# Kernel optimization log

Hardware: AMD Instinct MI355X
Metric: run time of the kernel (lower is better)

## Reference

```python
import jax, jax.numpy as jnp
import numpy as np

NEG_INF = float(np.finfo(np.float32).min)


def setup_inputs() -> dict:
    key = jax.random.key(0)
    k1, k2, k3 = jax.random.split(key, 3)
    n_context, d_model = 4096, 2048
    x = jax.random.normal(k1, (n_context, d_model), dtype=jnp.float32)
    # nn.Linear default init scale ~ 1/sqrt(fan_in); use small weights for numeric sanity
    W_qk = jax.random.normal(k2, (d_model, d_model), dtype=jnp.float32) / np.sqrt(d_model)
    W_ov = jax.random.normal(k3, (d_model, d_model), dtype=jnp.float32) / np.sqrt(d_model)
    return {"x": x, "W_qk": W_qk, "W_ov": W_ov}


def reference(x, W_qk, W_ov):
    # Faithful to: softmax(X @ W_qk.T @ X.T + causal_mask) @ X @ W_ov.T
    # (biases of the torch Linears are never used in forward)
    n = x.shape[0]
    q = x @ W_qk.T                      # [n, d]
    scores = q @ x.T                    # [n, n]  (no 1/sqrt(d) scaling, as in source)
    causal = jnp.tril(jnp.ones((n, n), dtype=bool))
    scores = jnp.where(causal, scores, NEG_INF)  # additive -inf mask equivalent
    attn = jax.nn.softmax(scores, axis=-1)       # [n, n]
    out = (attn @ x) @ W_ov.T                    # [n, d]
    return out
```

## Files before the change

kernel.cpp:

```cpp
#include <hip/hip_runtime.h>
#include <hip/hip_bf16.h>
#include <stdint.h>
#include <stddef.h>
#include <math.h>

typedef _Float16 f16;
typedef __attribute__((ext_vector_type(8))) _Float16 f16x8;
typedef __attribute__((ext_vector_type(4))) float    f32x4;

constexpr int BM = 128, BN = 128, BK = 64;

#define GLOAD_LDS16(gp, lp)                                        \
    __builtin_amdgcn_global_load_lds(                              \
        (const __attribute__((address_space(1))) unsigned int*)(gp),\
        (__attribute__((address_space(3))) unsigned int*)(lp), 16, 0, 0)

#define MFMA_TILE(AV, BV)                                                     \
    do {                                                                      \
        __builtin_amdgcn_s_setprio(1);                                        \
        _Pragma("unroll")                                                     \
        for (int mi_ = 0; mi_ < 4; ++mi_)                                     \
            _Pragma("unroll")                                                 \
            for (int ni_ = 0; ni_ < 4; ++ni_)                                 \
                acc[mi_][ni_] = __builtin_amdgcn_mfma_f32_16x16x32_f16(       \
                    (AV)[mi_], (BV)[ni_], acc[mi_][ni_], 0, 0, 0);            \
        __builtin_amdgcn_s_setprio(0);                                        \
    } while (0)

template <int EPI>
__global__ __launch_bounds__(512, 2) void gemm8_a2(
    const f16* __restrict__ Ah, const f16* __restrict__ Al,
    const f16* __restrict__ B,
    float* __restrict__ Cf, f16* __restrict__ Co, f16* __restrict__ Clo,
    int M, int N, int K)
{
    const int bx = blockIdx.x;
    const int by = blockIdx.y;

    const int tid   = threadIdx.x;
    const int lane  = tid & 63;
    const int wave  = tid >> 6;
    const int wm    = wave >> 2;
    const int wn    = wave & 3;
    const int lrow  = lane & 15;
    const int lquad = lane >> 4;

    __shared__ f16 lds[2][32768];

    const int row0 = by * 128;
    const int col0 = bx * 256;

    const int srow = tid >> 3;
    const int scol = ((tid & 7) ^ (srow & 7)) * 8;
    const int loff = wave * 512;

    const int g0 = ((lquad)     ^ (lrow & 7)) * 8;
    const int g1 = ((4 + lquad) ^ (lrow & 7)) * 8;

    const int arow = (wm * 64 + lrow) * 64;
    const int brow = (wn * 64 + lrow) * 64 + 16384;

    const f16* gAh = Ah + (size_t)(row0 + srow) * K + scol;
    const f16* gAl = Al + (size_t)(row0 + srow) * K + scol;
    const f16* gB  = B  + (size_t)(col0 + srow) * K + scol;
    const size_t r64 = (size_t)64 * K;

    f32x4 acc[4][4];
    const f32x4 fz = {0.f, 0.f, 0.f, 0.f};
    #pragma unroll
    for (int i = 0; i < 4; ++i)
        #pragma unroll
        for (int j = 0; j < 4; ++j) acc[i][j] = fz;

    const int nt = K / 64;

    #pragma unroll
    for (int u = 0; u < 4; ++u)
        GLOAD_LDS16(gB + u * r64, &lds[0][16384 + u * 4096 + loff]);
    #pragma unroll
    for (int u = 0; u < 2; ++u)
        GLOAD_LDS16(gAh + u * r64, &lds[0][u * 4096 + loff]);
    #pragma unroll
    for (int u = 0; u < 2; ++u)
        GLOAD_LDS16(gAl + u * r64, &lds[0][8192 + u * 4096 + loff]);
    asm volatile("s_waitcnt vmcnt(0)");
    __builtin_amdgcn_s_barrier();

    for (int t = 0; t < nt; ++t) {
        const f16* bufc = &lds[t & 1][0];
        f16* bufn = &lds[(t + 1) & 1][0];
        const bool stage = (t + 1 < nt);
        const size_t kn = (size_t)(t + 1) * 64;

        f16x8 ah0[4], ah1[4], al0[4], al1[4], bv0[4], bv1[4];

        #pragma unroll
        for (int mi = 0; mi < 4; ++mi)
            ah0[mi] = *(const f16x8*)&bufc[arow + mi * 1024 + g0];
        #pragma unroll
        for (int ni = 0; ni < 4; ++ni)
            bv0[ni] = *(const f16x8*)&bufc[brow + ni * 1024 + g0];
        #pragma unroll
        for (int mi = 0; mi < 4; ++mi)
            ah1[mi] = *(const f16x8*)&bufc[arow + mi * 1024 + g1];
        #pragma unroll
        for (int ni = 0; ni < 4; ++ni)
            bv1[ni] = *(const f16x8*)&bufc[brow + ni * 1024 + g1];
        #pragma unroll
        for (int mi = 0; mi < 4; ++mi)
            al0[mi] = *(const f16x8*)&bufc[8192 + arow + mi * 1024 + g0];
        #pragma unroll
        for (int mi = 0; mi < 4; ++mi)
            al1[mi] = *(const f16x8*)&bufc[8192 + arow + mi * 1024 + g1];

        if (stage) {
            GLOAD_LDS16(gB + kn,           &bufn[16384 + loff]);
            GLOAD_LDS16(gB + r64 + kn,     &bufn[16384 +  4096 + loff]);
            GLOAD_LDS16(gB + 2 * r64 + kn, &bufn[16384 +  8192 + loff]);
            GLOAD_LDS16(gB + 3 * r64 + kn, &bufn[16384 + 12288 + loff]);
            GLOAD_LDS16(gAh + kn,          &bufn[loff]);
            GLOAD_LDS16(gAh + r64 + kn,    &bufn[4096 + loff]);
            GLOAD_LDS16(gAl + kn,          &bufn[ 8192 + loff]);
            GLOAD_LDS16(gAl + r64 + kn,    &bufn[12288 + loff]);
        }

        MFMA_TILE(ah0, bv0);
        MFMA_TILE(ah1, bv1);
        MFMA_TILE(al0, bv0);
        MFMA_TILE(al1, bv1);

        asm volatile("s_waitcnt vmcnt(0)");
        __builtin_amdgcn_s_barrier();
    }

    #pragma unroll
    for (int mi = 0; mi < 4; ++mi) {
        #pragma unroll
        for (int ni = 0; ni < 4; ++ni) {
            #pragma unroll
            for (int r = 0; r < 4; ++r) {
                const int row = row0 + wm * 64 + mi * 16 + lquad * 4 + r;
                const int col = col0 + wn * 64 + ni * 16 + lrow;
                const size_t idx = (size_t)row * N + col;
                const float v = acc[mi][ni][r];
                if (EPI == 0) {
                    Cf[idx] = v;
                } else {
                    const f16 h = (f16)v;
                    Co[idx]  = h;
                    Clo[idx] = (f16)(v - (float)h);
                }
            }
        }
    }
}

__global__ __launch_bounds__(512, 2) void gemm8_s_jobs(
    const f16* __restrict__ Ah, const f16* __restrict__ Al,
    const f16* __restrict__ B,
    float* __restrict__ Cf, int N, int K)
{
    const int b = blockIdx.x;
    const int j = (b & 7) * 32 + (b >> 3);
    int r = (int)sqrtf((float)j);
    while (r * r > j) --r;
    while ((r + 1) * (r + 1) <= j) ++r;
    const int u = j - r * r;
    const int by = (u < r) ? 2 * r : 2 * r + 1;
    const int bx = (u < r) ? u : u - r;

    const int tid   = threadIdx.x;
    const int lane  = tid & 63;
    const int wave  = tid >> 6;
    const int wm    = wave >> 2;
    const int wn    = wave & 3;
    const int lrow  = lane & 15;
    const int lquad = lane >> 4;

    __shared__ f16 lds[2][32768];

    const int row0 = by * 128;
    const int col0 = bx * 256;

    const int srow = tid >> 3;
    const int scol = ((tid & 7) ^ (srow & 7)) * 8;
    const int loff = wave * 512;

    const int g0 = ((lquad)     ^ (lrow & 7)) * 8;
    const int g1 = ((4 + lquad) ^ (lrow & 7)) * 8;

    const int arow = (wm * 64 + lrow) * 64;
    const int brow = (wn * 64 + lrow) * 64 + 16384;

    const f16* gAh = Ah + (size_t)(row0 + srow) * K + scol;
    const f16* gAl = Al + (size_t)(row0 + srow) * K + scol;
    const f16* gB  = B  + (size_t)(col0 + srow) * K + scol;
    const size_t r64 = (size_t)64 * K;

    f32x4 acc[4][4];
    const f32x4 fz = {0.f, 0.f, 0.f, 0.f};
    #pragma unroll
    for (int i = 0; i < 4; ++i)
        #pragma unroll
        for (int jj = 0; jj < 4; ++jj) acc[i][jj] = fz;

    const int nt = K / 64;

    #pragma unroll
    for (int u2 = 0; u2 < 4; ++u2)
        GLOAD_LDS16(gB + u2 * r64, &lds[0][16384 + u2 * 4096 + loff]);
    #pragma unroll
    for (int u2 = 0; u2 < 2; ++u2)
        GLOAD_LDS16(gAh + u2 * r64, &lds[0][u2 * 4096 + loff]);
    #pragma unroll
    for (int u2 = 0; u2 < 2; ++u2)
        GLOAD_LDS16(gAl + u2 * r64, &lds[0][8192 + u2 * 4096 + loff]);
    asm volatile("s_waitcnt vmcnt(0)");
    __builtin_amdgcn_s_barrier();

    for (int t = 0; t < nt; ++t) {
        const f16* bufc = &lds[t & 1][0];
        f16* bufn = &lds[(t + 1) & 1][0];
        const bool stage = (t + 1 < nt);
        const size_t kn = (size_t)(t + 1) * 64;

        f16x8 ah0[4], ah1[4], al0[4], al1[4], bv0[4], bv1[4];

        #pragma unroll
        for (int mi = 0; mi < 4; ++mi)
            ah0[mi] = *(const f16x8*)&bufc[arow + mi * 1024 + g0];
        #pragma unroll
        for (int ni = 0; ni < 4; ++ni)
            bv0[ni] = *(const f16x8*)&bufc[brow + ni * 1024 + g0];
        #pragma unroll
        for (int mi = 0; mi < 4; ++mi)
            ah1[mi] = *(const f16x8*)&bufc[arow + mi * 1024 + g1];
        #pragma unroll
        for (int ni = 0; ni < 4; ++ni)
            bv1[ni] = *(const f16x8*)&bufc[brow + ni * 1024 + g1];
        #pragma unroll
        for (int mi = 0; mi < 4; ++mi)
            al0[mi] = *(const f16x8*)&bufc[8192 + arow + mi * 1024 + g0];
        #pragma unroll
        for (int mi = 0; mi < 4; ++mi)
            al1[mi] = *(const f16x8*)&bufc[8192 + arow + mi * 1024 + g1];

        if (stage) {
            GLOAD_LDS16(gB + kn,           &bufn[16384 + loff]);
            GLOAD_LDS16(gB + r64 + kn,     &bufn[16384 +  4096 + loff]);
            GLOAD_LDS16(gB + 2 * r64 + kn, &bufn[16384 +  8192 + loff]);
            GLOAD_LDS16(gB + 3 * r64 + kn, &bufn[16384 + 12288 + loff]);
            GLOAD_LDS16(gAh + kn,          &bufn[loff]);
            GLOAD_LDS16(gAh + r64 + kn,    &bufn[4096 + loff]);
            GLOAD_LDS16(gAl + kn,          &bufn[ 8192 + loff]);
            GLOAD_LDS16(gAl + r64 + kn,    &bufn[12288 + loff]);
        }

        MFMA_TILE(ah0, bv0);
        MFMA_TILE(ah1, bv1);
        MFMA_TILE(al0, bv0);
        MFMA_TILE(al1, bv1);

        asm volatile("s_waitcnt vmcnt(0)");
        __builtin_amdgcn_s_barrier();
    }

    #pragma unroll
    for (int mi = 0; mi < 4; ++mi) {
        #pragma unroll
        for (int ni = 0; ni < 4; ++ni) {
            #pragma unroll
            for (int rr = 0; rr < 4; ++rr) {
                const int row = row0 + wm * 64 + mi * 16 + lquad * 4 + rr;
                const int col = col0 + wn * 64 + ni * 16 + lrow;
                Cf[(size_t)row * N + col] = acc[mi][ni][rr];
            }
        }
    }
}

__global__ __launch_bounds__(256) void gemm_half_splitk(
    const f16* __restrict__ Ah, const f16* __restrict__ Al,
    const f16* __restrict__ B, float* __restrict__ Spart, int Kg)
{
    const int kc = blockIdx.x;
    const int h  = blockIdx.y;
    const int row0 = h * 256;
    const int kbeg = kc * 256;

    const int tid   = threadIdx.x;
    const int lane  = tid & 63;
    const int wave  = tid >> 6;
    const int wm    = wave >> 1;
    const int wn    = wave & 1;
    const int lrow  = lane & 15;
    const int lquad = lane >> 4;

    __shared__ f16 sAh[BM * BK];
    __shared__ f16 sAl[BM * BK];
    __shared__ f16 sB [BM * BK];

    const int srow = tid >> 3;
    const int scol = (((tid & 7) ^ ((tid >> 3) & 7))) * 8;
    const int lbase = wave * 512;

    f32x4 acc[4][4];
    const f32x4 fz = {0.f, 0.f, 0.f, 0.f};
    #pragma unroll
    for (int i = 0; i < 4; ++i)
        #pragma unroll
        for (int jj = 0; jj < 4; ++jj) acc[i][jj] = fz;

    for (int k0 = kbeg; k0 < kbeg + 256; k0 += BK) {
        __syncthreads();
        #pragma unroll
        for (int r = 0; r < 4; ++r) {
            const int trow = srow + 32 * r;
            const size_t ga = (size_t)(row0 + trow) * Kg + k0 + scol;
            const int ldst = lbase + r * 2048;
            GLOAD_LDS16(&Ah[ga], &sAh[ldst]);
            GLOAD_LDS16(&Al[ga], &sAl[ldst]);
            GLOAD_LDS16(&B [ga], &sB [ldst]);
        }
        __syncthreads();

        #pragma unroll
        for (int kk = 0; kk < 2; ++kk) {
            const int grpA = ((kk * 4 + lquad) ^ (lrow & 7)) * 8;
            f16x8 ah[4], al[4], bv[4];
            #pragma unroll
            for (int mi = 0; mi < 4; ++mi) {
                const int off = (wm * 64 + mi * 16 + lrow) * BK + grpA;
                ah[mi] = *reinterpret_cast<const f16x8*>(&sAh[off]);
                al[mi] = *reinterpret_cast<const f16x8*>(&sAl[off]);
            }
            #pragma unroll
            for (int ni = 0; ni < 4; ++ni)
                bv[ni] = *reinterpret_cast<const f16x8*>(
                    &sB[(wn * 64 + ni * 16 + lrow) * BK + grpA]);

            #pragma unroll
            for (int mi = 0; mi < 4; ++mi)
                #pragma unroll
                for (int ni = 0; ni < 4; ++ni) {
                    acc[mi][ni] = __builtin_amdgcn_mfma_f32_16x16x32_f16(
                        ah[mi], bv[ni], acc[mi][ni], 0, 0, 0);
                    acc[mi][ni] = __builtin_amdgcn_mfma_f32_16x16x32_f16(
                        al[mi], bv[ni], acc[mi][ni], 0, 0, 0);
                }
        }
    }

    float* outp = Spart + ((size_t)(kc * 16 + h)) * (128 * 128);
    #pragma unroll
    for (int mi = 0; mi < 4; ++mi) {
        #pragma unroll
        for (int ni = 0; ni < 4; ++ni) {
            #pragma unroll
            for (int r = 0; r < 4; ++r) {
                const int row = wm * 64 + mi * 16 + lquad * 4 + r;
                const int col = wn * 64 + ni * 16 + lrow;
                outp[row * 128 + col] = acc[mi][ni][r];
            }
        }
    }
}

__global__ __launch_bounds__(256) void combine_halves(
    const float* __restrict__ Spart, float* __restrict__ S, int n)
{
    const int h = blockIdx.y;
    const int e = (blockIdx.x * 256 + threadIdx.x) * 4;
    float4 a = *reinterpret_cast<const float4*>(
        &Spart[(size_t)h * (128 * 128) + e]);
    #pragma unroll
    for (int kc = 1; kc < 8; ++kc) {
        const float4 b = *reinterpret_cast<const float4*>(
            &Spart[(size_t)(kc * 16 + h) * (128 * 128) + e]);
        a.x += b.x; a.y += b.y; a.z += b.z; a.w += b.w;
    }
    const int i = e >> 7, jj = e & 127;
    *reinterpret_cast<float4*>(&S[(size_t)(h * 256 + i) * n + h * 256 + jj]) = a;
}

template <int EPI, bool KCAUSAL>
__global__ __launch_bounds__(512, 2) void gemm8_1t(
    const f16* __restrict__ A, const f16* __restrict__ B,
    float* __restrict__ Cf, f16* __restrict__ Co,
    int M, int N, int K)
{
    const int bx = blockIdx.x;
    const int by = KCAUSAL ? ((int)gridDim.y - 1 - (int)blockIdx.y) : blockIdx.y;

    const int tid   = threadIdx.x;
    const int lane  = tid & 63;
    const int wave  = tid >> 6;
    const int wm    = wave >> 2;
    const int wn    = wave & 3;
    const int lrow  = lane & 15;
    const int lquad = lane >> 4;

    __shared__ f16 lds[3][24576];

    const int row0 = by * 128;
    const int col0 = bx * 256;

    const int srow = tid >> 3;
    const int scol = ((tid & 7) ^ (srow & 7)) * 8;
    const int loff = wave * 512;
    const int g0 = ((lquad)     ^ (lrow & 7)) * 8;
    const int g1 = ((4 + lquad) ^ (lrow & 7)) * 8;
    const int arow = (wm * 64 + lrow) * 64;
    const int brow = (wn * 64 + lrow) * 64 + 8192;

    const f16* gA = A + (size_t)(row0 + srow) * K + scol;
    const f16* gB = B + (size_t)(col0 + srow) * K + scol;
    const size_t r64 = (size_t)64 * K;

    f32x4 acc[4][4];
    const f32x4 fz = {0.f, 0.f, 0.f, 0.f};
    #pragma unroll
    for (int i = 0; i < 4; ++i)
        #pragma unroll
        for (int j = 0; j < 4; ++j) acc[i][j] = fz;

    const int Keff = KCAUSAL ? (by + 1) * 128 : K;
    const int nt = Keff / 64;

    #pragma unroll
    for (int tt = 0; tt < 2; ++tt) {
        const size_t kk = (size_t)tt * 64;
        #pragma unroll
        for (int u = 0; u < 4; ++u)
            GLOAD_LDS16(gB + u * r64 + kk, &lds[tt][8192 + u * 4096 + loff]);
        #pragma unroll
        for (int u = 0; u < 2; ++u)
            GLOAD_LDS16(gA + u * r64 + kk, &lds[tt][u * 4096 + loff]);
    }
    asm volatile("s_waitcnt vmcnt(6)");
    __builtin_amdgcn_s_barrier();

    int cur = 0;
    for (int t = 0; t < nt; ++t) {
        const int nb = (cur >= 1) ? (cur - 1) : (cur + 2);
        const bool stage2 = (t + 2 < nt);
        const size_t kn = (size_t)(t + 2) * 64;
        const f16* bufc = &lds[cur][0];
        f16* bufn = &lds[nb][0];

        f16x8 av0[4], av1[4], bv0[4], bv1[4];

        #pragma unroll
        for (int mi = 0; mi < 4; ++mi)
            av0[mi] = *(const f16x8*)&bufc[arow + mi * 1024 + g0];
        #pragma unroll
        for (int ni = 0; ni < 4; ++ni)
            bv0[ni] = *(const f16x8*)&bufc[brow + ni * 1024 + g0];
        #pragma unroll
        for (int mi = 0; mi < 4; ++mi)
            av1[mi] = *(const f16x8*)&bufc[arow + mi * 1024 + g1];
        #pragma unroll
        for (int ni = 0; ni < 4; ++ni)
            bv1[ni] = *(const f16x8*)&bufc[brow + ni * 1024 + g1];

        if (stage2) {
            GLOAD_LDS16(gB + kn,           &bufn[8192 + loff]);
            GLOAD_LDS16(gB + r64 + kn,     &bufn[8192 +  4096 + loff]);
            GLOAD_LDS16(gB + 2 * r64 + kn, &bufn[8192 +  8192 + loff]);
            GLOAD_LDS16(gB + 3 * r64 + kn, &bufn[8192 + 12288 + loff]);
            GLOAD_LDS16(gA + kn,           &bufn[loff]);
            GLOAD_LDS16(gA + r64 + kn,     &bufn[4096 + loff]);
        }

        MFMA_TILE(av0, bv0);
        MFMA_TILE(av1, bv1);

        if (stage2) asm volatile("s_waitcnt vmcnt(6)");
        else        asm volatile("s_waitcnt vmcnt(0)");
        __builtin_amdgcn_s_barrier();

        cur = (cur == 2) ? 0 : cur + 1;
    }

    #pragma unroll
    for (int mi = 0; mi < 4; ++mi) {
        #pragma unroll
        for (int ni = 0; ni < 4; ++ni) {
            #pragma unroll
            for (int r = 0; r < 4; ++r) {
                const int row = row0 + wm * 64 + mi * 16 + lquad * 4 + r;
                const int col = col0 + wn * 64 + ni * 16 + lrow;
                const size_t idx = (size_t)row * N + col;
                const float v = acc[mi][ni][r];
                if (EPI == 0) Cf[idx] = v;
                else          Co[idx] = (f16)v;
            }
        }
    }
}

__global__ __launch_bounds__(256) void split_f32_f16(
    const float* __restrict__ in, f16* __restrict__ hi, f16* __restrict__ lo,
    size_t nelem)
{
    const size_t i = ((size_t)blockIdx.x * 256 + threadIdx.x) * 4;
    if (i >= nelem) return;
    const float4 v = *reinterpret_cast<const float4*>(in + i);
    union { f16 h[4]; ushort4 u; } H, L;
    H.h[0] = (f16)v.x; H.h[1] = (f16)v.y; H.h[2] = (f16)v.z; H.h[3] = (f16)v.w;
    *reinterpret_cast<ushort4*>(hi + i) = H.u;
    if (lo) {
        L.h[0] = (f16)(v.x - (float)H.h[0]);
        L.h[1] = (f16)(v.y - (float)H.h[1]);
        L.h[2] = (f16)(v.z - (float)H.h[2]);
        L.h[3] = (f16)(v.w - (float)H.h[3]);
        *reinterpret_cast<ushort4*>(lo + i) = L.u;
    }
}

__global__ __launch_bounds__(256) void prep_x(
    const float* __restrict__ in, f16* __restrict__ hi, f16* __restrict__ lo,
    f16* __restrict__ tr, int rows, int cols)
{
    __shared__ float tile[32][33];
    const int bx = blockIdx.x;
    const int by = blockIdx.y;
    const int tx = threadIdx.x & 31;
    const int ty = threadIdx.x >> 5;
    #pragma unroll
    for (int r = 0; r < 4; ++r) {
        const int row = by * 32 + ty + 8 * r;
        const int col = bx * 32 + tx;
        const float v = in[(size_t)row * cols + col];
        tile[ty + 8 * r][tx] = v;
        const f16 h = (f16)v;
        hi[(size_t)row * cols + col] = h;
        lo[(size_t)row * cols + col] = (f16)(v - (float)h);
    }
    __syncthreads();
    #pragma unroll
    for (int r = 0; r < 4; ++r)
        tr[(size_t)(bx * 32 + ty + 8 * r) * rows + by * 32 + tx] =
            (f16)tile[tx][ty + 8 * r];
}

__global__ __launch_bounds__(256) void softmax_rows(
    const float* __restrict__ S, f16* __restrict__ P, int n)
{
    const int row = blockIdx.x;
    const int len = row + 1;
    const int padlen = ((row >> 7) + 1) << 7;
    const float* srow = S + (size_t)row * n;
    f16* prow = P + (size_t)row * n;
    const int tid = threadIdx.x;
    const int lane = tid & 63, wave = tid >> 6;
    __shared__ float rowbuf[4096];
    __shared__ float redm[4], reds[4];

    float m = -3.0e38f, s = 0.f;
    for (int j = tid; j < len; j += 256) {
        const float v = srow[j];
        rowbuf[j] = v;
        const float mn = fmaxf(m, v);
        s = s * __expf(m - mn) + __expf(v - mn);
        m = mn;
    }
    #pragma unroll
    for (int off = 32; off; off >>= 1) {
        const float mo = __shfl_xor(m, off, 64);
        const float so = __shfl_xor(s, off, 64);
        const float mn = fmaxf(m, mo);
        s = s * __expf(m - mn) + so * __expf(mo - mn);
        m = mn;
    }
    if (lane == 0) { redm[wave] = m; reds[wave] = s; }
    __syncthreads();
    float M = redm[0], Sm = reds[0];
    #pragma unroll
    for (int w = 1; w < 4; ++w) {
        const float mn = fmaxf(M, redm[w]);
        Sm = Sm * __expf(M - mn) + reds[w] * __expf(redm[w] - mn);
        M = mn;
    }
    const float inv = 1.0f / Sm;

    const f16 z = (f16)0.0f;
    for (int j = tid; j < padlen; j += 256)
        prow[j] = (j < len) ? (f16)(__expf(rowbuf[j] - M) * inv) : z;
}

extern "C" void kernel_launch(void* const* d_in, const int* in_sizes, int n_in,
                              void* d_out, int out_size, void* d_ws, size_t ws_size,
                              hipStream_t stream)
{
    const int n = 4096, d = 2048;
    const float* x   = (const float*)d_in[0];
    const float* Wqk = (const float*)d_in[1];
    const float* Wov = (const float*)d_in[2];
    float* out = (float*)d_out;

    char* ws = (char*)d_ws;
    const size_t MB = 1 << 20;
    f16*   xh   = (f16*)  (ws);
    f16*   xl   = (f16*)  (ws + 16 * MB);
    f16*   Wh   = (f16*)  (ws + 32 * MB);
    f16*   Wovh = (f16*)  (ws + 40 * MB);
    f16*   xTh  = (f16*)  (ws + 48 * MB);
    f16*   qh   = (f16*)  (ws + 64 * MB);
    f16*   ql   = (f16*)  (ws + 80 * MB);
    float* S    = (float*)(ws + 96 * MB);
    float* Sp   = (float*)(ws + 16 * MB);
    f16*   P    = (f16*)  (ws);
    f16*   o    = (f16*)  (ws + 64 * MB);

    const dim3 blk(256);
    const dim3 blk8(512);

    split_f32_f16<<<dim3((d * d) / (256 * 4)), blk, 0, stream>>>(Wqk, Wh, nullptr, (size_t)d * d);
    split_f32_f16<<<dim3((d * d) / (256 * 4)), blk, 0, stream>>>(Wov, Wovh, nullptr, (size_t)d * d);
    prep_x<<<dim3(d / 32, n / 32), blk, 0, stream>>>(x, xh, xl, xTh, n, d);

    gemm8_a2<1><<<dim3(d / 256, n / 128), blk8, 0, stream>>>(
        xh, xl, Wh, nullptr, qh, ql, n, d, d);

    gemm8_s_jobs<<<dim3(256), blk8, 0, stream>>>(qh, ql, xh, S, n, d);
    gemm_half_splitk<<<dim3(8, 16), blk, 0, stream>>>(qh, ql, xh, Sp, d);
    combine_halves<<<dim3(16, 16), blk, 0, stream>>>(Sp, S, n);

    softmax_rows<<<dim3(n), blk, 0, stream>>>(S, P, n);

    gemm8_1t<2, true><<<dim3(d / 256, n / 128), blk8, 0, stream>>>(
        P, xTh, nullptr, o, n, d, n);

    gemm8_1t<0, false><<<dim3(d / 256, n / 128), blk8, 0, stream>>>(
        o, Wovh, out, nullptr, n, d, d);
}
```

Measured before the change: 365.9 us.

## Interleave MFMA with LDS reads, XCD-aware block remap, branchless prefetch

Moves the global-to-LDS prefetch earlier in each K iteration and interleaves the MFMA tiles with the LDS fragment reads. sched_group_barrier hints pin the order of MFMA, DS-read and VMEM instruction groups so loads overlap with matrix math. Workgroup IDs are remapped so consecutive tiles land on the same XCD, aiming for better L2 reuse in the non-causal GEMMs. The staging branch is removed by issuing redundant reloads of the last tile, which costs a little extra memory traffic and assumes the workgroup count is a multiple of 8.

```diff
diff --git a/kernel.cpp b/kernel.cpp
--- a/kernel.cpp
+++ b/kernel.cpp
@@ -27,6 +27,8 @@
         __builtin_amdgcn_s_setprio(0);                                        \
     } while (0)
 
+#define SGB __builtin_amdgcn_sched_group_barrier
+
 template <int EPI>
 __global__ __launch_bounds__(512, 2) void gemm8_a2(
     const f16* __restrict__ Ah, const f16* __restrict__ Al,
@@ -34,8 +36,13 @@
     float* __restrict__ Cf, f16* __restrict__ Co, f16* __restrict__ Clo,
     int M, int N, int K)
 {
-    const int bx = blockIdx.x;
-    const int by = blockIdx.y;
+    const int gx  = gridDim.x;
+    const int nwg = gx * gridDim.y;
+    const int id  = blockIdx.y * gx + blockIdx.x;
+    const int cpx = nwg >> 3;
+    const int j   = (id & 7) * cpx + (id >> 3);
+    const int bx  = j % gx;
+    const int by  = j / gx;
 
     const int tid   = threadIdx.x;
     const int lane  = tid & 63;
@@ -70,7 +77,7 @@
     #pragma unroll
     for (int i = 0; i < 4; ++i)
         #pragma unroll
-        for (int j = 0; j < 4; ++j) acc[i][j] = fz;
+        for (int jj = 0; jj < 4; ++jj) acc[i][jj] = fz;
 
     const int nt = K / 64;
 
@@ -89,8 +96,7 @@
     for (int t = 0; t < nt; ++t) {
         const f16* bufc = &lds[t & 1][0];
         f16* bufn = &lds[(t + 1) & 1][0];
-        const bool stage = (t + 1 < nt);
-        const size_t kn = (size_t)(t + 1) * 64;
+        const size_t kn = (size_t)((t + 1 < nt) ? t + 1 : t) * 64;
 
         f16x8 ah0[4], ah1[4], al0[4], al1[4], bv0[4], bv1[4];
 
@@ -100,34 +106,46 @@
         #pragma unroll
         for (int ni = 0; ni < 4; ++ni)
             bv0[ni] = *(const f16x8*)&bufc[brow + ni * 1024 + g0];
+
+        GLOAD_LDS16(gB + kn,           &bufn[16384 + loff]);
+        GLOAD_LDS16(gB + r64 + kn,     &bufn[16384 +  4096 + loff]);
+        GLOAD_LDS16(gB + 2 * r64 + kn, &bufn[16384 +  8192 + loff]);
+        GLOAD_LDS16(gB + 3 * r64 + kn, &bufn[16384 + 12288 + loff]);
+        GLOAD_LDS16(gAh + kn,          &bufn[loff]);
+        GLOAD_LDS16(gAh + r64 + kn,    &bufn[4096 + loff]);
+        GLOAD_LDS16(gAl + kn,          &bufn[ 8192 + loff]);
+        GLOAD_LDS16(gAl + r64 + kn,    &bufn[12288 + loff]);
+
         #pragma unroll
         for (int mi = 0; mi < 4; ++mi)
             ah1[mi] = *(const f16x8*)&bufc[arow + mi * 1024 + g1];
         #pragma unroll
         for (int ni = 0; ni < 4; ++ni)
             bv1[ni] = *(const f16x8*)&bufc[brow + ni * 1024 + g1];
+
+        MFMA_TILE(ah0, bv0);
+
         #pragma unroll
         for (int mi = 0; mi < 4; ++mi)
             al0[mi] = *(const f16x8*)&bufc[8192 + arow + mi * 1024 + g0];
+
+        MFMA_TILE(ah1, bv1);
+
         #pragma unroll
         for (int mi = 0; mi < 4; ++mi)
             al1[mi] = *(const f16x8*)&bufc[8192 + arow + mi * 1024 + g1];
 
-        if (stage) {
-            GLOAD_LDS16(gB + kn,           &bufn[16384 + loff]);
-            GLOAD_LDS16(gB + r64 + kn,     &bufn[16384 +  4096 + loff]);
-            GLOAD_LDS16(gB + 2 * r64 + kn, &bufn[16384 +  8192 + loff]);
-            GLOAD_LDS16(gB + 3 * r64 + kn, &bufn[16384 + 12288 + loff]);
-            GLOAD_LDS16(gAh + kn,          &bufn[loff]);
-            GLOAD_LDS16(gAh + r64 + kn,    &bufn[4096 + loff]);
-            GLOAD_LDS16(gAl + kn,          &bufn[ 8192 + loff]);
-            GLOAD_LDS16(gAl + r64 + kn,    &bufn[12288 + loff]);
-        }
-
-        MFMA_TILE(ah0, bv0);
-        MFMA_TILE(ah1, bv1);
         MFMA_TILE(al0, bv0);
         MFMA_TILE(al1, bv1);
+
+        SGB(0x100, 8, 0);
+        SGB(0x20,  8, 0);
+        SGB(0x100, 8, 0);
+        SGB(0x8,  16, 0);
+        SGB(0x100, 4, 0);
+        SGB(0x8,  16, 0);
+        SGB(0x100, 4, 0);
+        SGB(0x8,  32, 0);
 
         asm volatile("s_waitcnt vmcnt(0)");
         __builtin_amdgcn_s_barrier();
@@ -221,8 +239,7 @@
     for (int t = 0; t < nt; ++t) {
         const f16* bufc = &lds[t & 1][0];
         f16* bufn = &lds[(t + 1) & 1][0];
-        const bool stage = (t + 1 < nt);
-        const size_t kn = (size_t)(t + 1) * 64;
+        const size_t kn = (size_t)((t + 1 < nt) ? t + 1 : t) * 64;
 
         f16x8 ah0[4], ah1[4], al0[4], al1[4], bv0[4], bv1[4];
 
@@ -232,34 +249,46 @@
         #pragma unroll
         for (int ni = 0; ni < 4; ++ni)
             bv0[ni] = *(const f16x8*)&bufc[brow + ni * 1024 + g0];
+
+        GLOAD_LDS16(gB + kn,           &bufn[16384 + loff]);
+        GLOAD_LDS16(gB + r64 + kn,     &bufn[16384 +  4096 + loff]);
+        GLOAD_LDS16(gB + 2 * r64 + kn, &bufn[16384 +  8192 + loff]);
+        GLOAD_LDS16(gB + 3 * r64 + kn, &bufn[16384 + 12288 + loff]);
+        GLOAD_LDS16(gAh + kn,          &bufn[loff]);
+        GLOAD_LDS16(gAh + r64 + kn,    &bufn[4096 + loff]);
+        GLOAD_LDS16(gAl + kn,          &bufn[ 8192 + loff]);
+        GLOAD_LDS16(gAl + r64 + kn,    &bufn[12288 + loff]);
+
         #pragma unroll
         for (int mi = 0; mi < 4; ++mi)
             ah1[mi] = *(const f16x8*)&bufc[arow + mi * 1024 + g1];
         #pragma unroll
         for (int ni = 0; ni < 4; ++ni)
             bv1[ni] = *(const f16x8*)&bufc[brow + ni * 1024 + g1];
+
+        MFMA_TILE(ah0, bv0);
+
         #pragma unroll
         for (int mi = 0; mi < 4; ++mi)
             al0[mi] = *(const f16x8*)&bufc[8192 + arow + mi * 1024 + g0];
+
+        MFMA_TILE(ah1, bv1);
+
         #pragma unroll
         for (int mi = 0; mi < 4; ++mi)
             al1[mi] = *(const f16x8*)&bufc[8192 + arow + mi * 1024 + g1];
 
-        if (stage) {
-            GLOAD_LDS16(gB + kn,           &bufn[16384 + loff]);
-            GLOAD_LDS16(gB + r64 + kn,     &bufn[16384 +  4096 + loff]);
-            GLOAD_LDS16(gB + 2 * r64 + kn, &bufn[16384 +  8192 + loff]);
-            GLOAD_LDS16(gB + 3 * r64 + kn, &bufn[16384 + 12288 + loff]);
-            GLOAD_LDS16(gAh + kn,          &bufn[loff]);
-            GLOAD_LDS16(gAh + r64 + kn,    &bufn[4096 + loff]);
-            GLOAD_LDS16(gAl + kn,          &bufn[ 8192 + loff]);
-            GLOAD_LDS16(gAl + r64 + kn,    &bufn[12288 + loff]);
-        }
-
-        MFMA_TILE(ah0, bv0);
-        MFMA_TILE(ah1, bv1);
         MFMA_TILE(al0, bv0);
         MFMA_TILE(al1, bv1);
+
+        SGB(0x100, 8, 0);
+        SGB(0x20,  8, 0);
+        SGB(0x100, 8, 0);
+        SGB(0x8,  16, 0);
+        SGB(0x100, 4, 0);
+        SGB(0x8,  16, 0);
+        SGB(0x100, 4, 0);
+        SGB(0x8,  32, 0);
 
         asm volatile("s_waitcnt vmcnt(0)");
         __builtin_amdgcn_s_barrier();
@@ -389,8 +418,19 @@
     float* __restrict__ Cf, f16* __restrict__ Co,
     int M, int N, int K)
 {
-    const int bx = blockIdx.x;
-    const int by = KCAUSAL ? ((int)gridDim.y - 1 - (int)blockIdx.y) : blockIdx.y;
+    int bx, by;
+    if (KCAUSAL) {
+        bx = blockIdx.x;
+        by = (int)gridDim.y - 1 - (int)blockIdx.y;
+    } else {
+        const int gx  = gridDim.x;
+        const int nwg = gx * gridDim.y;
+        const int id  = blockIdx.y * gx + blockIdx.x;
+        const int cpx = nwg >> 3;
+        const int j   = (id & 7) * cpx + (id >> 3);
+        bx = j % gx;
+        by = j / gx;
+    }
 
     const int tid   = threadIdx.x;
     const int lane  = tid & 63;
@@ -422,7 +462,7 @@
     #pragma unroll
     for (int i = 0; i < 4; ++i)
         #pragma unroll
-        for (int j = 0; j < 4; ++j) acc[i][j] = fz;
+        for (int j2 = 0; j2 < 4; ++j2) acc[i][j2] = fz;
 
     const int Keff = KCAUSAL ? (by + 1) * 128 : K;
     const int nt = Keff / 64;
@@ -443,8 +483,7 @@
     int cur = 0;
     for (int t = 0; t < nt; ++t) {
         const int nb = (cur >= 1) ? (cur - 1) : (cur + 2);
-        const bool stage2 = (t + 2 < nt);
-        const size_t kn = (size_t)(t + 2) * 64;
+        const size_t kn = (size_t)((t + 2 < nt) ? t + 2 : nt - 1) * 64;
         const f16* bufc = &lds[cur][0];
         f16* bufn = &lds[nb][0];
 
@@ -456,6 +495,14 @@
         #pragma unroll
         for (int ni = 0; ni < 4; ++ni)
             bv0[ni] = *(const f16x8*)&bufc[brow + ni * 1024 + g0];
+
+        GLOAD_LDS16(gB + kn,           &bufn[8192 + loff]);
+        GLOAD_LDS16(gB + r64 + kn,     &bufn[8192 +  4096 + loff]);
+        GLOAD_LDS16(gB + 2 * r64 + kn, &bufn[8192 +  8192 + loff]);
+        GLOAD_LDS16(gB + 3 * r64 + kn, &bufn[8192 + 12288 + loff]);
+        GLOAD_LDS16(gA + kn,           &bufn[loff]);
+        GLOAD_LDS16(gA + r64 + kn,     &bufn[4096 + loff]);
+
         #pragma unroll
         for (int mi = 0; mi < 4; ++mi)
             av1[mi] = *(const f16x8*)&bufc[arow + mi * 1024 + g1];
@@ -463,20 +510,15 @@
         for (int ni = 0; ni < 4; ++ni)
             bv1[ni] = *(const f16x8*)&bufc[brow + ni * 1024 + g1];
 
-        if (stage2) {
-            GLOAD_LDS16(gB + kn,           &bufn[8192 + loff]);
-            GLOAD_LDS16(gB + r64 + kn,     &bufn[8192 +  4096 + loff]);
-            GLOAD_LDS16(gB + 2 * r64 + kn, &bufn[8192 +  8192 + loff]);
-            GLOAD_LDS16(gB + 3 * r64 + kn, &bufn[8192 + 12288 + loff]);
-            GLOAD_LDS16(gA + kn,           &bufn[loff]);
-            GLOAD_LDS16(gA + r64 + kn,     &bufn[4096 + loff]);
-        }
-
         MFMA_TILE(av0, bv0);
         MFMA_TILE(av1, bv1);
 
-        if (stage2) asm volatile("s_waitcnt vmcnt(6)");
-        else        asm volatile("s_waitcnt vmcnt(0)");
+        SGB(0x100, 8, 0);
+        SGB(0x20,  6, 0);
+        SGB(0x100, 8, 0);
+        SGB(0x8,  32, 0);
+
+        asm volatile("s_waitcnt vmcnt(6)");
         __builtin_amdgcn_s_barrier();
 
         cur = (cur == 2) ? 0 : cur + 1;
```

Result: no change. 367.2 us (+0.4%).

## Triple-buffer A tiles and split K-step into two barrier-fenced MFMA phases

Applied to the files above, without the earlier changes.

Both GEMM kernels now keep A (hi/lo) in a three-deep LDS ring and B in a two-deep ring. A is prefetched two k-steps ahead and B one step ahead, and each k-step is split into two half-phases with barriers and a partial vmcnt wait, so global loads stay in flight across MFMA work. The generic GEMM also remaps workgroup IDs so that consecutive IDs are spread in an XCD-aware order to improve L2 locality. LDS use grows from 128KB to 160KB per block, which can lower occupancy below the two blocks per CU that the launch bounds assume. The extra barriers per iteration add synchronisation overhead.

```diff
diff --git a/kernel.cpp b/kernel.cpp
--- a/kernel.cpp
+++ b/kernel.cpp
@@ -34,8 +34,13 @@
     float* __restrict__ Cf, f16* __restrict__ Co, f16* __restrict__ Clo,
     int M, int N, int K)
 {
-    const int bx = blockIdx.x;
-    const int by = blockIdx.y;
+    const int gx  = gridDim.x;
+    const int nwg = gx * gridDim.y;
+    const int id  = blockIdx.y * gx + blockIdx.x;
+    const int cpx = nwg >> 3;
+    const int j   = (id & 7) * cpx + (id >> 3);
+    const int bx  = j % gx;
+    const int by  = j / gx;
 
     const int tid   = threadIdx.x;
     const int lane  = tid & 63;
@@ -45,7 +50,8 @@
     const int lrow  = lane & 15;
     const int lquad = lane >> 4;
 
-    __shared__ f16 lds[2][32768];
+    __shared__ f16 ldsA[3][16384];
+    __shared__ f16 ldsB[2][16384];
 
     const int row0 = by * 128;
     const int col0 = bx * 256;
@@ -58,7 +64,7 @@
     const int g1 = ((4 + lquad) ^ (lrow & 7)) * 8;
 
     const int arow = (wm * 64 + lrow) * 64;
-    const int brow = (wn * 64 + lrow) * 64 + 16384;
+    const int brow = (wn * 64 + lrow) * 64;
 
     const f16* gAh = Ah + (size_t)(row0 + srow) * K + scol;
     const f16* gAl = Al + (size_t)(row0 + srow) * K + scol;
@@ -70,67 +76,76 @@
     #pragma unroll
     for (int i = 0; i < 4; ++i)
         #pragma unroll
-        for (int j = 0; j < 4; ++j) acc[i][j] = fz;
+        for (int jj = 0; jj < 4; ++jj) acc[i][jj] = fz;
 
     const int nt = K / 64;
 
+    GLOAD_LDS16(gAh,       &ldsA[0][loff]);
+    GLOAD_LDS16(gAh + r64, &ldsA[0][4096 + loff]);
+    GLOAD_LDS16(gAl,       &ldsA[0][8192 + loff]);
+    GLOAD_LDS16(gAl + r64, &ldsA[0][12288 + loff]);
     #pragma unroll
     for (int u = 0; u < 4; ++u)
-        GLOAD_LDS16(gB + u * r64, &lds[0][16384 + u * 4096 + loff]);
-    #pragma unroll
-    for (int u = 0; u < 2; ++u)
-        GLOAD_LDS16(gAh + u * r64, &lds[0][u * 4096 + loff]);
-    #pragma unroll
-    for (int u = 0; u < 2; ++u)
-        GLOAD_LDS16(gAl + u * r64, &lds[0][8192 + u * 4096 + loff]);
-    asm volatile("s_waitcnt vmcnt(0)");
+        GLOAD_LDS16(gB + u * r64, &ldsB[0][u * 4096 + loff]);
+    GLOAD_LDS16(gAh + 64,       &ldsA[1][loff]);
+    GLOAD_LDS16(gAh + r64 + 64, &ldsA[1][4096 + loff]);
+    GLOAD_LDS16(gAl + 64,       &ldsA[1][8192 + loff]);
+    GLOAD_LDS16(gAl + r64 + 64, &ldsA[1][12288 + loff]);
+    asm volatile("s_waitcnt vmcnt(4)");
     __builtin_amdgcn_s_barrier();
 
+    int aidx = 0;
     for (int t = 0; t < nt; ++t) {
-        const f16* bufc = &lds[t & 1][0];
-        f16* bufn = &lds[(t + 1) & 1][0];
-        const bool stage = (t + 1 < nt);
-        const size_t kn = (size_t)(t + 1) * 64;
-
-        f16x8 ah0[4], ah1[4], al0[4], al1[4], bv0[4], bv1[4];
-
-        #pragma unroll
-        for (int mi = 0; mi < 4; ++mi)
-            ah0[mi] = *(const f16x8*)&bufc[arow + mi * 1024 + g0];
+        const f16* bA = &ldsA[aidx][0];
+        const f16* bB = &ldsB[t & 1][0];
+        f16* nA = &ldsA[(aidx + 2 >= 3) ? aidx - 1 : aidx + 2][0];
+        f16* nB = &ldsB[(t + 1) & 1][0];
+        const size_t kB1 = (size_t)((t + 1 < nt) ? t + 1 : nt - 1) * 64;
+        const size_t kA2 = (size_t)((t + 2 < nt) ? t + 2 : nt - 1) * 64;
+
+        f16x8 ah0[4], al0[4], bv0[4], ah1[4], al1[4], bv1[4];
+
+        #pragma unroll
+        for (int mi = 0; mi < 4; ++mi)
+            ah0[mi] = *(const f16x8*)&bA[arow + mi * 1024 + g0];
         #pragma unroll
         for (int ni = 0; ni < 4; ++ni)
-            bv0[ni] = *(const f16x8*)&bufc[brow + ni * 1024 + g0];
-        #pragma unroll
-        for (int mi = 0; mi < 4; ++mi)
-            ah1[mi] = *(const f16x8*)&bufc[arow + mi * 1024 + g1];
+            bv0[ni] = *(const f16x8*)&bB[brow + ni * 1024 + g0];
+        #pragma unroll
+        for (int mi = 0; mi < 4; ++mi)
+            al0[mi] = *(const f16x8*)&bA[8192 + arow + mi * 1024 + g0];
+
+        #pragma unroll
+        for (int u = 0; u < 4; ++u)
+            GLOAD_LDS16(gB + u * r64 + kB1, &nB[u * 4096 + loff]);
+
+        __builtin_amdgcn_s_barrier();
+        MFMA_TILE(ah0, bv0);
+        MFMA_TILE(al0, bv0);
+        __builtin_amdgcn_s_barrier();
+
+        #pragma unroll
+        for (int mi = 0; mi < 4; ++mi)
+            ah1[mi] = *(const f16x8*)&bA[arow + mi * 1024 + g1];
         #pragma unroll
         for (int ni = 0; ni < 4; ++ni)
-            bv1[ni] = *(const f16x8*)&bufc[brow + ni * 1024 + g1];
-        #pragma unroll
-        for (int mi = 0; mi < 4; ++mi)
-            al0[mi] = *(const f16x8*)&bufc[8192 + arow + mi * 1024 + g0];
-        #pragma unroll
-        for (int mi = 0; mi < 4; ++mi)
-            al1[mi] = *(const f16x8*)&bufc[8192 + arow + mi * 1024 + g1];
-
-        if (stage) {
-            GLOAD_LDS16(gB + kn,           &bufn[16384 + loff]);
-            GLOAD_LDS16(gB + r64 + kn,     &bufn[16384 +  4096 + loff]);
-            GLOAD_LDS16(gB + 2 * r64 + kn, &bufn[16384 +  8192 + loff]);
-            GLOAD_LDS16(gB + 3 * r64 + kn, &bufn[16384 + 12288 + loff]);
-            GLOAD_LDS16(gAh + kn,          &bufn[loff]);
-            GLOAD_LDS16(gAh + r64 + kn,    &bufn[4096 + loff]);
-            GLOAD_LDS16(gAl + kn,          &bufn[ 8192 + loff]);
-            GLOAD_LDS16(gAl + r64 + kn,    &bufn[12288 + loff]);
-        }
-
-        MFMA_TILE(ah0, bv0);
+            bv1[ni] = *(const f16x8*)&bB[brow + ni * 1024 + g1];
+        #pragma unroll
+        for (int mi = 0; mi < 4; ++mi)
+            al1[mi] = *(const f16x8*)&bA[8192 + arow + mi * 1024 + g1];
+
+        GLOAD_LDS16(gAh + kA2,       &nA[loff]);
+        GLOAD_LDS16(gAh + r64 + kA2, &nA[4096 + loff]);
+        GLOAD_LDS16(gAl + kA2,       &nA[8192 + loff]);
+        GLOAD_LDS16(gAl + r64 + kA2, &nA[12288 + loff]);
+
+        asm volatile("s_waitcnt vmcnt(4)");
+        __builtin_amdgcn_s_barrier();
         MFMA_TILE(ah1, bv1);
-        MFMA_TILE(al0, bv0);
         MFMA_TILE(al1, bv1);
-
-        asm volatile("s_waitcnt vmcnt(0)");
-        __builtin_amdgcn_s_barrier();
+        __builtin_amdgcn_s_barrier();
+
+        aidx = (aidx == 2) ? 0 : aidx + 1;
     }
 
     #pragma unroll
@@ -177,7 +192,8 @@
     const int lrow  = lane & 15;
     const int lquad = lane >> 4;
 
-    __shared__ f16 lds[2][32768];
+    __shared__ f16 ldsA[3][16384];
+    __shared__ f16 ldsB[2][16384];
 
     const int row0 = by * 128;
     const int col0 = bx * 256;
@@ -190,7 +206,7 @@
     const int g1 = ((4 + lquad) ^ (lrow & 7)) * 8;
 
     const int arow = (wm * 64 + lrow) * 64;
-    const int brow = (wn * 64 + lrow) * 64 + 16384;
+    const int brow = (wn * 64 + lrow) * 64;
 
     const f16* gAh = Ah + (size_t)(row0 + srow) * K + scol;
     const f16* gAl = Al + (size_t)(row0 + srow) * K + scol;
@@ -206,63 +222,72 @@
 
     const int nt = K / 64;
 
+    GLOAD_LDS16(gAh,       &ldsA[0][loff]);
+    GLOAD_LDS16(gAh + r64, &ldsA[0][4096 + loff]);
+    GLOAD_LDS16(gAl,       &ldsA[0][8192 + loff]);
+    GLOAD_LDS16(gAl + r64, &ldsA[0][12288 + loff]);
     #pragma unroll
     for (int u2 = 0; u2 < 4; ++u2)
-        GLOAD_LDS16(gB + u2 * r64, &lds[0][16384 + u2 * 4096 + loff]);
-    #pragma unroll
-    for (int u2 = 0; u2 < 2; ++u2)
-        GLOAD_LDS16(gAh + u2 * r64, &lds[0][u2 * 4096 + loff]);
-    #pragma unroll
-    for (int u2 = 0; u2 < 2; ++u2)
-        GLOAD_LDS16(gAl + u2 * r64, &lds[0][8192 + u2 * 4096 + loff]);
-    asm volatile("s_waitcnt vmcnt(0)");
+        GLOAD_LDS16(gB + u2 * r64, &ldsB[0][u2 * 4096 + loff]);
+    GLOAD_LDS16(gAh + 64,       &ldsA[1][loff]);
+    GLOAD_LDS16(gAh + r64 + 64, &ldsA[1][4096 + loff]);
+    GLOAD_LDS16(gAl + 64,       &ldsA[1][8192 + loff]);
+    GLOAD_LDS16(gAl + r64 + 64, &ldsA[1][12288 + loff]);
+    asm volatile("s_waitcnt vmcnt(4)");
     __builtin_amdgcn_s_barrier();
 
+    int aidx = 0;
     for (int t = 0; t < nt; ++t) {
-        const f16* bufc = &lds[t & 1][0];
-        f16* bufn = &lds[(t + 1) & 1][0];
-        const bool stage = (t + 1 < nt);
-        const size_t kn = (size_t)(t + 1) * 64;
-
-        f16x8 ah0[4], ah1[4], al0[4], al1[4], bv0[4], bv1[4];
-
-        #pragma unroll
-        for (int mi = 0; mi < 4; ++mi)
-            ah0[mi] = *(const f16x8*)&bufc[arow + mi * 1024 + g0];
+        const f16* bA = &ldsA[aidx][0];
+        const f16* bB = &ldsB[t & 1][0];
+        f16* nA = &ldsA[(aidx + 2 >= 3) ? aidx - 1 : aidx + 2][0];
+        f16* nB = &ldsB[(t + 1) & 1][0];
+        const size_t kB1 = (size_t)((t + 1 < nt) ? t + 1 : nt - 1) * 64;
+        const size_t kA2 = (size_t)((t + 2 < nt) ? t + 2 : nt - 1) * 64;
+
+        f16x8 ah0[4], al0[4], bv0[4], ah1[4], al1[4], bv1[4];
+
+        #pragma unroll
+        for (int mi = 0; mi < 4; ++mi)
+            ah0[mi] = *(const f16x8*)&bA[arow + mi * 1024 + g0];
         #pragma unroll
         for (int ni = 0; ni < 4; ++ni)
-            bv0[ni] = *(const f16x8*)&bufc[brow + ni * 1024 + g0];
-        #pragma unroll
-        for (int mi = 0; mi < 4; ++mi)
-            ah1[mi] = *(const f16x8*)&bufc[arow + mi * 1024 + g1];
+            bv0[ni] = *(const f16x8*)&bB[brow + ni * 1024 + g0];
+        #pragma unroll
+        for (int mi = 0; mi < 4; ++mi)
+            al0[mi] = *(const f16x8*)&bA[8192 + arow + mi * 1024 + g0];
+
+        #pragma unroll
+        for (int u2 = 0; u2 < 4; ++u2)
+            GLOAD_LDS16(gB + u2 * r64 + kB1, &nB[u2 * 4096 + loff]);
+
+        __builtin_amdgcn_s_barrier();
+        MFMA_TILE(ah0, bv0);
+        MFMA_TILE(al0, bv0);
+        __builtin_amdgcn_s_barrier();
+
+        #pragma unroll
+        for (int mi = 0; mi < 4; ++mi)
+            ah1[mi] = *(const f16x8*)&bA[arow + mi * 1024 + g1];
         #pragma unroll
         for (int ni = 0; ni < 4; ++ni)
-            bv1[ni] = *(const f16x8*)&bufc[brow + ni * 1024 + g1];
-        #pragma unroll
-        for (int mi = 0; mi < 4; ++mi)
-            al0[mi] = *(const f16x8*)&bufc[8192 + arow + mi * 1024 + g0];
-        #pragma unroll
-        for (int mi = 0; mi < 4; ++mi)
-            al1[mi] = *(const f16x8*)&bufc[8192 + arow + mi * 1024 + g1];
-
-        if (stage) {
-            GLOAD_LDS16(gB + kn,           &bufn[16384 + loff]);
-            GLOAD_LDS16(gB + r64 + kn,     &bufn[16384 +  4096 + loff]);
-            GLOAD_LDS16(gB + 2 * r64 + kn, &bufn[16384 +  8192 + loff]);
-            GLOAD_LDS16(gB + 3 * r64 + kn, &bufn[16384 + 12288 + loff]);
-            GLOAD_LDS16(gAh + kn,          &bufn[loff]);
-            GLOAD_LDS16(gAh + r64 + kn,    &bufn[4096 + loff]);
-            GLOAD_LDS16(gAl + kn,          &bufn[ 8192 + loff]);
-            GLOAD_LDS16(gAl + r64 + kn,    &bufn[12288 + loff]);
-        }
-
-        MFMA_TILE(ah0, bv0);
+            bv1[ni] = *(const f16x8*)&bB[brow + ni * 1024 + g1];
+        #pragma unroll
+        for (int mi = 0; mi < 4; ++mi)
+            al1[mi] = *(const f16x8*)&bA[8192 + arow + mi * 1024 + g1];
+
+        GLOAD_LDS16(gAh + kA2,       &nA[loff]);
+        GLOAD_LDS16(gAh + r64 + kA2, &nA[4096 + loff]);
+        GLOAD_LDS16(gAl + kA2,       &nA[8192 + loff]);
+        GLOAD_LDS16(gAl + r64 + kA2, &nA[12288 + loff]);
+
+        asm volatile("s_waitcnt vmcnt(4)");
+        __builtin_amdgcn_s_barrier();
         MFMA_TILE(ah1, bv1);
-        MFMA_TILE(al0, bv0);
         MFMA_TILE(al1, bv1);
-
-        asm volatile("s_waitcnt vmcnt(0)");
-        __builtin_amdgcn_s_barrier();
+        __builtin_amdgcn_s_barrier();
+
+        aidx = (aidx == 2) ? 0 : aidx + 1;
     }
 
     #pragma unroll
```

Measured after the change: 362.2 us. About the same (-1.0%).
